# Kernel tuning notes

Measured on AMD Instinct MI355X. Metric: run time of the kernel, lower is better.

Reference implementation:

```python
import jax, jax.numpy as jnp
import numpy as np

EPS = 0.05      # entropic regularization, matches eps arg in forward
ITERS = 100     # Sinkhorn fixed-point iterations (auction analog; converged math)

def setup_inputs() -> dict:
    key = jax.random.key(0)
    k1, k2 = jax.random.split(key)
    B, N, D = 16, 2048, 3
    x = jax.random.uniform(k1, (B, N, D), dtype=jnp.float32)
    y = jax.random.uniform(k2, (B, N, D), dtype=jnp.float32)
    return {"x": x, "y": y}

def _emd_mean(x, y):
    # pairwise squared distances: [B, N, N]
    x2 = jnp.sum(x * x, axis=-1)                      # [B, N]
    y2 = jnp.sum(y * y, axis=-1)                      # [B, N]
    xy = jnp.einsum('bnd,bmd->bnm', x, y)             # [B, N, N]
    C = x2[:, :, None] + y2[:, None, :] - 2.0 * xy
    C = jnp.maximum(C, 0.0)

    B, N, _ = C.shape
    logK = -C / EPS                                   # [B, N, N]
    log_mu = jnp.full((B, N), -jnp.log(jnp.float32(N)))
    log_nu = log_mu

    def body(carry, _):
        f, g = carry
        # f_i = eps*(log mu_i - logsumexp_j((g_j - C_ij)/eps))
        f = EPS * (log_mu - jax.nn.logsumexp(logK + (g / EPS)[:, None, :], axis=2))
        g = EPS * (log_nu - jax.nn.logsumexp(logK + (f / EPS)[:, :, None], axis=1))
        return (f, g), None

    f0 = jnp.zeros((B, N), dtype=C.dtype)
    g0 = jnp.zeros((B, N), dtype=C.dtype)
    (f, g), _ = jax.lax.scan(body, (f0, g0), None, length=ITERS)

    # transport plan P_ij = exp((f_i + g_j - C_ij)/eps) (already includes mu,nu)
    logP = (f[:, :, None] + g[:, None, :] - C) / EPS
    P = jnp.exp(logP)
    # per-source-point matched squared distance, scaled by N (row mass = 1/N)
    dis = jnp.sum(P * C, axis=2) * N                  # [B, N]
    return dis.mean()

def reference(x, y):
    return _emd_mean(x, y)
```

## Files before the change

kernel.cpp:

```cpp
#include <hip/hip_runtime.h>

#define BB 16
#define NN 2048
#define NITERS 100

#define K2E      28.853900817779268f
#define TWO_K2E  57.707801635558536f
#define INV2K    0.017328679513998632f
#define INV_K2E  0.034657359027997264f
#define INV4K    0.008664339756999316f
#define LMU      (-11.0f)

#if __has_builtin(__builtin_amdgcn_exp2f)
#define EXP2F(x) __builtin_amdgcn_exp2f(x)
#else
#define EXP2F(x) exp2f(x)
#endif

typedef float v2f __attribute__((ext_vector_type(2)));
typedef float v4f __attribute__((ext_vector_type(4)));

#define DSTORE(p, v) __hip_atomic_store((p), (v), __ATOMIC_RELAXED, __HIP_MEMORY_SCOPE_AGENT)
#define DLOAD(p)     __hip_atomic_load((p), __ATOMIC_RELAXED, __HIP_MEMORY_SCOPE_AGENT)

__device__ __forceinline__ float bfly8(const float acc[8], int lane) {
    const bool b0 = lane & 1, b1 = lane & 2, b2 = lane & 4;
    float v4[4], v2_[2], v1;
    #pragma unroll
    for (int i = 0; i < 4; ++i) {
        float recv = __shfl_xor(b0 ? acc[i] : acc[i+4], 1, 64);
        v4[i] = (b0 ? acc[i+4] : acc[i]) + recv;
    }
    #pragma unroll
    for (int i = 0; i < 2; ++i) {
        float recv = __shfl_xor(b1 ? v4[i] : v4[i+2], 2, 64);
        v2_[i] = (b1 ? v4[i+2] : v4[i]) + recv;
    }
    {
        float recv = __shfl_xor(b2 ? v2_[0] : v2_[1], 4, 64);
        v1 = (b2 ? v2_[1] : v2_[0]) + recv;
    }
    v1 += __shfl_xor(v1, 8, 64);
    v1 += __shfl_xor(v1, 16, 64);
    v1 += __shfl_xor(v1, 32, 64);
    return v1;
}

__device__ __forceinline__ float sumpassF(
    const v4f* __restrict__ U, const v4f* __restrict__ T,
    const float* __restrict__ sdv,
    int rloc, int lane)
{
    v2f xp0[4], xp1[4], xp2[4], acc2[4];
    #pragma unroll
    for (int p = 0; p < 4; ++p) {
        const v4f ua = U[rloc + 2*p];
        const v4f ub = U[rloc + 2*p + 1];
        xp0[p] = (v2f){ua.x * INV2K, ub.x * INV2K};
        xp1[p] = (v2f){ua.y * INV2K, ub.y * INV2K};
        xp2[p] = (v2f){ua.z * INV2K, ub.z * INV2K};
        acc2[p] = (v2f){0.f, 0.f};
    }
    #pragma unroll 4
    for (int s = 0; s < 32; ++s) {
        const int p = lane + (s << 6);
        const v4f t = T[p];
        const float ad = sdv[p];
        const v2f a0v = (v2f){t.x, t.x}, a1v = (v2f){t.y, t.y};
        const v2f a2v = (v2f){t.z, t.z}, adv = (v2f){ad, ad};
        #pragma unroll
        for (int qq = 0; qq < 4; ++qq) {
            v2f d = __builtin_elementwise_fma(xp0[qq], a0v,
                    __builtin_elementwise_fma(xp1[qq], a1v,
                    __builtin_elementwise_fma(xp2[qq], a2v, adv)));
            acc2[qq] += (v2f){EXP2F(d.x), EXP2F(d.y)};
        }
    }
    float acc[8];
    #pragma unroll
    for (int p = 0; p < 4; ++p) { acc[2*p] = acc2[p].x; acc[2*p+1] = acc2[p].y; }
    return bfly8(acc, lane);
}

__device__ __forceinline__ float epilA(
    const v4f* __restrict__ U, const v4f* __restrict__ T,
    const float* __restrict__ gB,
    float Aval, int rloc, int jh, int lane)
{
    const int jb = (jh << 10) + lane;
    float dv[16];
    #pragma unroll
    for (int s = 0; s < 16; ++s)
        dv[s] = DLOAD(gB + jb + (s << 6));

    float xr0[8], xr1[8], xr2[8], Ak[8], x2k[8];
    #pragma unroll
    for (int k = 0; k < 8; ++k) {
        const v4f u = U[rloc + k];
        xr0[k] = u.x * INV2K;
        xr1[k] = u.y * INV2K;
        xr2[k] = u.z * INV2K;
        const int src = ((k & 1) << 2) | (k & 2) | ((k >> 2) & 1);
        Ak[k]  = __shfl(Aval, src, 64);
        x2k[k] = K2E * (xr0[k]*xr0[k] + xr1[k]*xr1[k] + xr2[k]*xr2[k]);
    }
    float acc = 0.f;
    for (int s = 0; s < 16; ++s) {
        const v4f t = T[jb + (s << 6)];
        const float a0 = t.x, a1 = t.y, a2 = t.z, tb = dv[s];
        const float q2 = (a0*a0 + a1*a1 + a2*a2) * INV4K;
        #pragma unroll
        for (int k = 0; k < 8; ++k) {
            float d = fmaf(xr0[k], a0, fmaf(xr1[k], a1, fmaf(xr2[k], a2, tb)));
            float P = EXP2F(d + Ak[k]);
            float C = fmaxf((x2k[k] + q2 - (d - tb)) * INV_K2E, 0.f);
            acc = fmaf(P, C, acc);
        }
    }
    return acc;
}

__global__ __launch_bounds__(1024, 4) void emd_sinkhornP(
    const float* __restrict__ x, const float* __restrict__ y,
    float* __restrict__ Af, float* __restrict__ Bf,
    int* __restrict__ flags, float* __restrict__ out)
{
    extern __shared__ float S[];
    __shared__ float wsum[16];

    const int tid  = threadIdx.x;
    const int lane = tid & 63;
    const int w    = tid >> 6;
    const int blk  = blockIdx.x;
    const int b    = blk >> 4;
    const int q    = blk & 15;
    const int base = b * NN;
    const int row0 = q * 128;
    const int rloc = row0 + w * 8;
    int* fb = flags + b * 64;

    v4f   *sy = (v4f*)S;
    v4f   *sx = (v4f*)S + NN;
    float *sd = (float*)((v4f*)S + 2 * NN);

    #pragma unroll
    for (int v = 0; v < 2; ++v) {
        const int p = tid + (v << 10);
        const float* px = x + 3 * (size_t)(base + p);
        sx[p] = (v4f){TWO_K2E * px[0], TWO_K2E * px[1], TWO_K2E * px[2], 0.f};
        const float* py = y + 3 * (size_t)(base + p);
        sy[p] = (v4f){TWO_K2E * py[0], TWO_K2E * py[1], TWO_K2E * py[2], 0.f};
    }
    if (tid < 128) {
        const int col = row0 + tid;
        const float* py = y + 3 * (size_t)(base + col);
        const float a = py[0], bb = py[1], c = py[2];
        DSTORE(&Bf[base + col], -K2E * (a*a + bb*bb + c*c));
    }

    #define PWS(pval, tgt, gsrc) do {                                           \
        __syncthreads();          \
        if (tid == 0)                                                           \
            __hip_atomic_store(fb + q * 4, (pval), __ATOMIC_RELEASE,            \
                               __HIP_MEMORY_SCOPE_AGENT);                       \
        for (;;) {                                                              \
            int vv = (lane < 16)                                                \
                ? __hip_atomic_load(fb + lane * 4, __ATOMIC_RELAXED,            \
                                    __HIP_MEMORY_SCOPE_AGENT)                   \
                : 0x7fffffff;                                                   \
            if (__ballot(vv >= (tgt)) == ~0ULL) break;                          \
            __builtin_amdgcn_s_sleep(1);                                        \
        }                                                                       \
        {                                   \
            const int o_ = (w << 7) + lane;                                     \
            float a_ = DLOAD((gsrc) + o_);                                      \
            float b_ = DLOAD((gsrc) + o_ + 64);                                 \
            sd[o_] = a_; sd[o_ + 64] = b_;                                      \
        }                                                                       \
        __syncthreads();                                       \
    } while (0)

    const int rr = ((lane & 1) << 2) | (lane & 2) | ((lane >> 2) & 1);
    float Aval = 0.f;

    PWS(1, 1, Bf + base);

    for (int it = 0; it < NITERS; ++it) {
        {
            float v1 = sumpassF(sx, sy, sd, rloc, lane);
            Aval = LMU - __log2f(v1);
            if (lane < 8) DSTORE(&Af[base + rloc + rr], Aval);
        }
        PWS(2 * it + 2, 2 * it + 2, Af + base);
        {
            float v1 = sumpassF(sy, sx, sd, rloc, lane);
            if (lane < 8)
                DSTORE(&Bf[base + rloc + rr], LMU - __log2f(v1));
        }
        PWS(2 * it + 3, 2 * it + 3, Bf + base);
    }

    {
        float s = epilA(sx, sy, Bf + base, Aval, rloc, 0, lane)
                + epilA(sx, sy, Bf + base, Aval, rloc, 1, lane);
        #pragma unroll
        for (int m = 32; m > 0; m >>= 1) s += __shfl_xor(s, m, 64);
        if (lane == 0) wsum[w] = s;
        __syncthreads();
        if (tid == 0) {
            float t = 0.f;
            #pragma unroll
            for (int i = 0; i < 16; ++i) t += wsum[i];
            atomicAdd(out, t * (1.0f / (float)BB));
        }
    }
    #undef PWS
}

__global__ __launch_bounds__(1024, 4) void emd_sinkhornU(
    const float* __restrict__ x, const float* __restrict__ y,
    float* __restrict__ Af, float* __restrict__ Bf,
    int* __restrict__ flags, float* __restrict__ out)
{
    extern __shared__ float S[];
    __shared__ float wsum[16];

    const int tid  = threadIdx.x;
    const int lane = tid & 63;
    const int w    = tid >> 6;
    const int blk  = blockIdx.x;
    const int b    = blk >> 4;
    const int q    = blk & 15;
    const int base = b * NN;
    const int row0 = q * 128;
    const int rloc = row0 + w * 8;
    int* fb = flags + 2048 + b * 64;

    v4f   *sy = (v4f*)S;
    v4f   *sx = (v4f*)S + NN;
    float *sd = (float*)((v4f*)S + 2 * NN);

    #pragma unroll
    for (int v = 0; v < 2; ++v) {
        const int p = tid + (v << 10);
        const float* px = x + 3 * (size_t)(base + p);
        sx[p] = (v4f){TWO_K2E * px[0], TWO_K2E * px[1], TWO_K2E * px[2], 0.f};
        const float* py = y + 3 * (size_t)(base + p);
        sy[p] = (v4f){TWO_K2E * py[0], TWO_K2E * py[1], TWO_K2E * py[2], 0.f};
    }
    if (tid < 128) {
        const int col = row0 + tid;
        const float* py = y + 3 * (size_t)(base + col);
        const float a = py[0], bb = py[1], c = py[2];
        DSTORE(&Bf[base + col], -K2E * (a*a + bb*bb + c*c));
    }
    __syncthreads();
    if (tid == 0)
        __hip_atomic_store(fb + q * 4, 1, __ATOMIC_RELEASE, __HIP_MEMORY_SCOPE_AGENT);

    #define WAITB2(tgt) do { __syncthreads();                                   \
        if (w == 0) {                                                           \
            for (;;) {                                                          \
                int vv = (lane < 16)                                            \
                    ? __hip_atomic_load(fb + lane * 4, __ATOMIC_RELAXED,        \
                                        __HIP_MEMORY_SCOPE_AGENT)               \
                    : 0x7fffffff;                                               \
                if (__ballot(vv >= (tgt)) == ~0ULL) break;                      \
                __builtin_amdgcn_s_sleep(1);                                    \
            }                                                                   \
        }                                                                       \
        __syncthreads(); } while (0)

    #define POSTB2(pval) do { __syncthreads();                                  \
        if (tid == 0)                                                           \
            __hip_atomic_store(fb + q * 4, (pval), __ATOMIC_RELEASE,            \
                               __HIP_MEMORY_SCOPE_AGENT);                       \
    } while (0)

    #define STAGE2(gsrc) do {                                                   \
        float t0_ = DLOAD((gsrc) + tid);                                        \
        float t1_ = DLOAD((gsrc) + tid + 1024);                                 \
        sd[tid] = t0_; sd[tid + 1024] = t1_;                                    \
        __syncthreads(); } while (0)

    WAITB2(1);

    const int rr = ((lane & 1) << 2) | (lane & 2) | ((lane >> 2) & 1);
    float Aval = 0.f;

    for (int it = 0; it < NITERS; ++it) {
        STAGE2(Bf + base);
        {
            float v1 = sumpassF(sx, sy, sd, rloc, lane);
            Aval = LMU - __log2f(v1);
            if (lane < 8) DSTORE(&Af[base + rloc + rr], Aval);
        }
        POSTB2(2 * it + 2);
        WAITB2(2 * it + 2);
        STAGE2(Af + base);
        {
            float v1 = sumpassF(sy, sx, sd, rloc, lane);
            if (lane < 8)
                DSTORE(&Bf[base + rloc + rr], LMU - __log2f(v1));
        }
        POSTB2(2 * it + 3);
        WAITB2(2 * it + 3);
    }

    {
        float s = epilA(sx, sy, Bf + base, Aval, rloc, 0, lane)
                + epilA(sx, sy, Bf + base, Aval, rloc, 1, lane);
        #pragma unroll
        for (int m = 32; m > 0; m >>= 1) s += __shfl_xor(s, m, 64);
        if (lane == 0) wsum[w] = s;
        __syncthreads();
        if (tid == 0) {
            float t = 0.f;
            #pragma unroll
            for (int i = 0; i < 16; ++i) t += wsum[i];
            atomicAdd(out, t * (1.0f / (float)BB));
        }
    }
    #undef WAITB2
    #undef POSTB2
    #undef STAGE2
}

extern "C" void kernel_launch(void* const* d_in, const int* in_sizes, int n_in,
                              void* d_out, int out_size, void* d_ws, size_t ws_size,
                              hipStream_t stream) {
    const float* x = (const float*)d_in[0];
    const float* y = (const float*)d_in[1];
    float* out = (float*)d_out;
    char* ws = (char*)d_ws;

    int*   flags = (int*)ws;
    float* Af    = (float*)(ws + 16384);
    float* Bf    = (float*)(ws + 16384 + (size_t)BB*NN*sizeof(float));

    hipMemsetAsync(flags, 0, 16384, stream);
    hipMemsetAsync(out, 0, sizeof(float), stream);

    void* args[] = {(void*)&x, (void*)&y, (void*)&Af, (void*)&Bf,
                    (void*)&flags, (void*)&out};

    const size_t shmem = (size_t)(2 * NN * 4 + NN) * sizeof(float);
    hipError_t ep = hipFuncSetAttribute((const void*)emd_sinkhornP,
                        hipFuncAttributeMaxDynamicSharedMemorySize, (int)shmem);
    hipError_t e = (ep == hipSuccess)
        ? hipLaunchCooperativeKernel((const void*)emd_sinkhornP,
                                     dim3(256), dim3(1024), args, shmem, stream)
        : hipErrorInvalidValue;
    if (e != hipSuccess) {
        hipError_t eu = hipFuncSetAttribute((const void*)emd_sinkhornU,
                            hipFuncAttributeMaxDynamicSharedMemorySize, (int)shmem);
        hipError_t e2 = (eu == hipSuccess)
            ? hipLaunchCooperativeKernel((const void*)emd_sinkhornU,
                                         dim3(256), dim3(1024), args, shmem, stream)
            : hipErrorInvalidValue;
        if (e2 != hipSuccess) {
            hipLaunchKernelGGL(emd_sinkhornU, dim3(256), dim3(1024), shmem,
                               stream, x, y, Af, Bf, flags, out);
        }
    }
}
```

Before: 2.528 ms.

## Split inter-block barrier into half-waits overlapping compute with producer blocks

The full 16-block spin barrier before each half-iteration is replaced by two partial waits. Each wait covers the 8 blocks producing one half of the dual vector, so a block can start its exp-sum over the first 1024 columns while the other half is still being written. Only wave 0 polls the flags and then releases the block through __syncthreads, and a final wait before the epilogue makes sure the last Bf update is visible. This is meant to shorten time spent stalled on the slowest block, at the cost of an extra block barrier per half and finer-grained flag polling.

After: 2.360 ms. 6.7% less time.

```diff
diff --git a/kernel.cpp b/kernel.cpp
--- a/kernel.cpp
+++ b/kernel.cpp
@@ -44,6 +44,60 @@
     v1 += __shfl_xor(v1, 16, 64);
     v1 += __shfl_xor(v1, 32, 64);
     return v1;
+}
+
+__device__ __forceinline__ float passH(
+    const v4f* __restrict__ U, const v4f* __restrict__ T,
+    const float* __restrict__ gsrc, float* __restrict__ sd,
+    int* __restrict__ fb, int tgt, int rloc, int lane, int w, int tid)
+{
+    v2f xp0[4], xp1[4], xp2[4], acc2[4];
+    #pragma unroll
+    for (int p = 0; p < 4; ++p) {
+        const v4f ua = U[rloc + 2*p];
+        const v4f ub = U[rloc + 2*p + 1];
+        xp0[p] = (v2f){ua.x * INV2K, ub.x * INV2K};
+        xp1[p] = (v2f){ua.y * INV2K, ub.y * INV2K};
+        xp2[p] = (v2f){ua.z * INV2K, ub.z * INV2K};
+        acc2[p] = (v2f){0.f, 0.f};
+    }
+    #pragma unroll
+    for (int hh = 0; hh < 2; ++hh) {
+        if (w == 0) {
+            for (;;) {
+                int vv = (lane < 8)
+                    ? __hip_atomic_load(fb + ((hh << 3) + lane) * 4,
+                                        __ATOMIC_RELAXED,
+                                        __HIP_MEMORY_SCOPE_AGENT)
+                    : 0x7fffffff;
+                if (__ballot(vv >= tgt) == ~0ULL) break;
+                __builtin_amdgcn_s_sleep(1);
+            }
+        }
+        __syncthreads();
+        sd[(hh << 10) + tid] = DLOAD(gsrc + (hh << 10) + tid);
+        __syncthreads();
+        const int sbase = hh << 4;
+        #pragma unroll 4
+        for (int s = sbase; s < sbase + 16; ++s) {
+            const int p = lane + (s << 6);
+            const v4f t = T[p];
+            const float ad = sd[p];
+            const v2f a0v = (v2f){t.x, t.x}, a1v = (v2f){t.y, t.y};
+            const v2f a2v = (v2f){t.z, t.z}, adv = (v2f){ad, ad};
+            #pragma unroll
+            for (int qq = 0; qq < 4; ++qq) {
+                v2f d = __builtin_elementwise_fma(xp0[qq], a0v,
+                        __builtin_elementwise_fma(xp1[qq], a1v,
+                        __builtin_elementwise_fma(xp2[qq], a2v, adv)));
+                acc2[qq] += (v2f){EXP2F(d.x), EXP2F(d.y)};
+            }
+        }
+    }
+    float acc[8];
+    #pragma unroll
+    for (int p = 0; p < 4; ++p) { acc[2*p] = acc2[p].x; acc[2*p+1] = acc2[p].y; }
+    return bfly8(acc, lane);
 }
 
 __device__ __forceinline__ float sumpassF(
@@ -120,7 +174,7 @@
     return acc;
 }
 
-__global__ __launch_bounds__(1024, 4) void emd_sinkhornP(
+__global__ __launch_bounds__(1024, 4) void emd_sinkhornHK(
     const float* __restrict__ x, const float* __restrict__ y,
     float* __restrict__ Af, float* __restrict__ Bf,
     int* __restrict__ flags, float* __restrict__ out)
@@ -158,47 +212,44 @@
         DSTORE(&Bf[base + col], -K2E * (a*a + bb*bb + c*c));
     }
 
-    #define PWS(pval, tgt, gsrc) do {                                           \
-        __syncthreads();          \
+    #define POSTH(pval) do { __syncthreads();                                   \
         if (tid == 0)                                                           \
             __hip_atomic_store(fb + q * 4, (pval), __ATOMIC_RELEASE,            \
                                __HIP_MEMORY_SCOPE_AGENT);                       \
-        for (;;) {                                                              \
-            int vv = (lane < 16)                                                \
-                ? __hip_atomic_load(fb + lane * 4, __ATOMIC_RELAXED,            \
-                                    __HIP_MEMORY_SCOPE_AGENT)                   \
-                : 0x7fffffff;                                                   \
-            if (__ballot(vv >= (tgt)) == ~0ULL) break;                          \
-            __builtin_amdgcn_s_sleep(1);                                        \
-        }                                                                       \
-        {                                   \
-            const int o_ = (w << 7) + lane;                                     \
-            float a_ = DLOAD((gsrc) + o_);                                      \
-            float b_ = DLOAD((gsrc) + o_ + 64);                                 \
-            sd[o_] = a_; sd[o_ + 64] = b_;                                      \
-        }                                                                       \
-        __syncthreads();                                       \
     } while (0)
+
+    POSTH(1);
 
     const int rr = ((lane & 1) << 2) | (lane & 2) | ((lane >> 2) & 1);
     float Aval = 0.f;
 
-    PWS(1, 1, Bf + base);
-
     for (int it = 0; it < NITERS; ++it) {
         {
-            float v1 = sumpassF(sx, sy, sd, rloc, lane);
+            float v1 = passH(sx, sy, Bf + base, sd, fb, 2 * it + 1,
+                             rloc, lane, w, tid);
             Aval = LMU - __log2f(v1);
             if (lane < 8) DSTORE(&Af[base + rloc + rr], Aval);
         }
-        PWS(2 * it + 2, 2 * it + 2, Af + base);
+        POSTH(2 * it + 2);
         {
-            float v1 = sumpassF(sy, sx, sd, rloc, lane);
+            float v1 = passH(sy, sx, Af + base, sd, fb, 2 * it + 2,
+                             rloc, lane, w, tid);
             if (lane < 8)
                 DSTORE(&Bf[base + rloc + rr], LMU - __log2f(v1));
         }
-        PWS(2 * it + 3, 2 * it + 3, Bf + base);
-    }
+        POSTH(2 * it + 3);
+    }
+    if (w == 0) {
+        for (;;) {
+            int vv = (lane < 16)
+                ? __hip_atomic_load(fb + lane * 4, __ATOMIC_RELAXED,
+                                    __HIP_MEMORY_SCOPE_AGENT)
+                : 0x7fffffff;
+            if (__ballot(vv >= 2 * NITERS + 1) == ~0ULL) break;
+            __builtin_amdgcn_s_sleep(1);
+        }
+    }
+    __syncthreads();
 
     {
         float s = epilA(sx, sy, Bf + base, Aval, rloc, 0, lane)
@@ -214,7 +265,7 @@
             atomicAdd(out, t * (1.0f / (float)BB));
         }
     }
-    #undef PWS
+    #undef POSTH
 }
 
 __global__ __launch_bounds__(1024, 4) void emd_sinkhornU(
@@ -345,10 +396,10 @@
                     (void*)&flags, (void*)&out};
 
     const size_t shmem = (size_t)(2 * NN * 4 + NN) * sizeof(float);
-    hipError_t ep = hipFuncSetAttribute((const void*)emd_sinkhornP,
+    hipError_t eh = hipFuncSetAttribute((const void*)emd_sinkhornHK,
                         hipFuncAttributeMaxDynamicSharedMemorySize, (int)shmem);
-    hipError_t e = (ep == hipSuccess)
-        ? hipLaunchCooperativeKernel((const void*)emd_sinkhornP,
+    hipError_t e = (eh == hipSuccess)
+        ? hipLaunchCooperativeKernel((const void*)emd_sinkhornHK,
                                      dim3(256), dim3(1024), args, shmem, stream)
         : hipErrorInvalidValue;
     if (e != hipSuccess) {
```
